# Performance work log

Measured on AMD Instinct MI355X. Metric: run time of the kernel, lower is better.

Reference implementation:

```python
import jax, jax.numpy as jnp
import numpy as np

B, S, H = 2, 2048, 2048
NH, NKV, HD = 16, 4, 128
LAT = H // 8  # compression_ratio=8


def _rope_tables():
    inv_freq = 1.0 / (10000.0 ** (jnp.arange(0, HD, 2, dtype=jnp.float32) / HD))
    pos = jnp.arange(S, dtype=jnp.float32)
    freqs = pos[:, None] * inv_freq[None, :]          # [S, HD/2]
    emb = jnp.concatenate([freqs, freqs], axis=-1)    # [S, HD]
    return jnp.cos(emb)[None, None], jnp.sin(emb)[None, None]  # [1,1,S,HD]


def setup_inputs() -> dict:
    key = jax.random.key(0)
    ks = jax.random.split(key, 8)
    std = 0.02
    hidden_states = jax.random.normal(ks[0], (B, S, H), dtype=jnp.float32)
    cos, sin = _rope_tables()
    # additive causal mask, broadcast over batch/heads
    causal = jnp.tril(jnp.ones((S, S), dtype=bool))
    attention_mask = jnp.where(causal, 0.0, -1e9).astype(jnp.float32)[None, None]
    Wq = jax.random.normal(ks[1], (H, H), dtype=jnp.float32) * std
    Wk = jax.random.normal(ks[2], (NKV * HD, H), dtype=jnp.float32) * std
    Wv = jax.random.normal(ks[3], (NKV * HD, H), dtype=jnp.float32) * std
    Wo = jax.random.normal(ks[4], (H, H), dtype=jnp.float32) * std
    Wl_in = jax.random.normal(ks[5], (LAT, H), dtype=jnp.float32) * std
    Wl_out = jax.random.normal(ks[6], (H, LAT), dtype=jnp.float32) * std
    latent_gate = jnp.ones((1,), dtype=jnp.float32)
    return dict(hidden_states=hidden_states, cos=cos, sin=sin,
                attention_mask=attention_mask, Wq=Wq, Wk=Wk, Wv=Wv, Wo=Wo,
                Wl_in=Wl_in, Wl_out=Wl_out, latent_gate=latent_gate)


def _rotate_half(x):
    x1, x2 = jnp.split(x, 2, axis=-1)
    return jnp.concatenate([-x2, x1], axis=-1)


def reference(hidden_states, cos, sin, attention_mask, Wq, Wk, Wv, Wo,
              Wl_in, Wl_out, latent_gate):
    b, s, h = hidden_states.shape
    # projections (torch Linear: x @ W.T)
    q = (hidden_states @ Wq.T).reshape(b, s, NH, HD).transpose(0, 2, 1, 3)    # [b,nh,s,hd]
    k = (hidden_states @ Wk.T).reshape(b, s, NKV, HD).transpose(0, 2, 1, 3)   # [b,nkv,s,hd]
    v = (hidden_states @ Wv.T).reshape(b, s, NKV, HD).transpose(0, 2, 1, 3)
    # inline RoPE
    c, sn = cos[:, :, :s, :], sin[:, :, :s, :]
    q = q * c + _rotate_half(q) * sn
    k = k * c + _rotate_half(k) * sn
    # GQA: replicate kv heads (repeat_interleave along head dim)
    rep = NH // NKV
    k = jnp.repeat(k, rep, axis=1)
    v = jnp.repeat(v, rep, axis=1)
    scores = jnp.einsum('bhqd,bhkd->bhqk', q, k) / np.sqrt(HD).astype(np.float32)
    scores = scores + attention_mask
    attn = jax.nn.softmax(scores, axis=-1)
    ctx = jnp.einsum('bhqk,bhkd->bhqd', attn, v)          # [b,nh,s,hd]
    ctx = ctx.transpose(0, 2, 1, 3).reshape(b, s, h)
    attn_out = ctx @ Wo.T
    latent = (hidden_states @ Wl_in.T) @ Wl_out.T          # low-rank residual branch
    return attn_out + latent_gate * latent
```

## Files before the change

kernel.cpp:

```cpp
#include <hip/hip_runtime.h>
#include <hip/hip_bf16.h>

#define Bn   2
#define Sn   2048
#define Hn   2048
#define NHn  16
#define NKVn 4
#define HDn  128
#define LATn 256
#define Mn   (Bn*Sn)
#define KC   2304

typedef unsigned short ushort_t;
typedef __attribute__((ext_vector_type(8))) short bf16x8;
typedef __attribute__((ext_vector_type(8))) unsigned short ushort8;
typedef __attribute__((ext_vector_type(4))) float f32x4;

__device__ __forceinline__ ushort_t f2bf(float f) {
    unsigned u = __float_as_uint(f);
    u += 0x7fffu + ((u >> 16) & 1u);
    return (ushort_t)(u >> 16);
}
__device__ __forceinline__ float bf2f(ushort_t h) {
    return __uint_as_float(((unsigned)h) << 16);
}
__device__ __forceinline__ void async16(const void* g, void* l) {
    __builtin_amdgcn_global_load_lds(
        (__attribute__((address_space(1))) void*)g,
        (__attribute__((address_space(3))) void*)l, 16, 0, 0);
}

struct CastArgs {
    const float* src[7];
    ushort_t*    dst[7];
    int n4[7];
    int sshift[7];
    int dcols[7];
    int dcoff[7];
};
__global__ __launch_bounds__(256)
void cast_fused(CastArgs a)
{
    int off = blockIdx.x * 256 + threadIdx.x;
    int seg = 0;
    while (seg < 6 && off >= a.n4[seg]) { off -= a.n4[seg]; ++seg; }
    const int r = off >> a.sshift[seg];
    const int c = off & ((1 << a.sshift[seg]) - 1);
    float4 f = ((const float4*)a.src[seg])[off];
    ushort4 o;
    o.x = f2bf(f.x); o.y = f2bf(f.y); o.z = f2bf(f.z); o.w = f2bf(f.w);
    ((ushort4*)a.dst[seg])[(size_t)r * a.dcols[seg] + a.dcoff[seg] + c] = o;
}

#define GEMM_BK64_LOOP(Aptr, Astr, Wptr, Wstr, Kdim)                          \
    for (int k0 = 0; k0 < (Kdim); k0 += 64) {                                 \
        _Pragma("unroll")                                                     \
        for (int it = 0; it < 4; ++it)                                        \
            async16((Aptr) + (size_t)(m0 + it*32 + srow)*(Astr) + k0 + scol,  \
                    As + (it*256 + tid)*8);                                   \
        _Pragma("unroll")                                                     \
        for (int it = 0; it < 4; ++it)                                        \
            async16((Wptr) + (size_t)(n0 + it*32 + srow)*(Wstr) + k0 + scol,  \
                    Bsm + (it*256 + tid)*8);                                  \
        __syncthreads();                                                      \
        _Pragma("unroll")                                                     \
        for (int hf = 0; hf < 2; ++hf) {                                      \
            bf16x8 af[4], bfr[4];                                             \
            _Pragma("unroll")                                                 \
            for (int mi = 0; mi < 4; ++mi)                                    \
                af[mi] = *(const bf16x8*)(As + aoff[hf*4 + mi]);              \
            _Pragma("unroll")                                                 \
            for (int ni = 0; ni < 4; ++ni)                                    \
                bfr[ni] = *(const bf16x8*)(Bsm + boff[hf*4 + ni]);            \
            _Pragma("unroll")                                                 \
            for (int mi = 0; mi < 4; ++mi)                                    \
                _Pragma("unroll")                                             \
                for (int ni = 0; ni < 4; ++ni)                                \
                    acc[mi][ni] = __builtin_amdgcn_mfma_f32_16x16x32_bf16(    \
                        af[mi], bfr[ni], acc[mi][ni], 0, 0, 0);               \
        }                                                                     \
        __syncthreads();                                                      \
    }

#define GEMM_COMMON_DECLS                                                     \
    const int tid  = threadIdx.x;                                             \
    const int lane = tid & 63, w = tid >> 6;                                  \
    const int t = lane & 15, q = lane >> 4;                                   \
    const int wm = w & 1, wn = w >> 1;                                        \
    const int srow = tid >> 3;                                                \
    const int scol = ((tid & 7) ^ ((tid >> 3) & 7)) * 8;                      \
    int aoff[8], boff[8];                                                     \
    _Pragma("unroll")                                                         \
    for (int hf = 0; hf < 2; ++hf)                                            \
        _Pragma("unroll")                                                     \
        for (int i = 0; i < 4; ++i) {                                         \
            aoff[hf*4 + i] = (wm*64 + i*16 + t)*64 + (((hf*4 + q) ^ (t & 7)) << 3); \
            boff[hf*4 + i] = (wn*64 + i*16 + t)*64 + (((hf*4 + q) ^ (t & 7)) << 3); \
        }                                                                     \
    f32x4 acc[4][4];                                                          \
    _Pragma("unroll")                                                         \
    for (int i = 0; i < 4; ++i)                                               \
        _Pragma("unroll")                                                     \
        for (int j = 0; j < 4; ++j) acc[i][j] = (f32x4){0.f, 0.f, 0.f, 0.f};

__global__ __launch_bounds__(256)
void gemm_qkv(const ushort_t* __restrict__ A, const ushort_t* __restrict__ W,
              ushort_t* __restrict__ qo, ushort_t* __restrict__ ko,
              ushort_t* __restrict__ vo)
{
    __shared__ __align__(16) ushort_t smem[16384];
    ushort_t* As  = smem;
    ushort_t* Bsm = smem + 8192;

    const int m0 = blockIdx.y * 128, n0 = blockIdx.x * 128;
    GEMM_COMMON_DECLS
    GEMM_BK64_LOOP(A, Hn, W, Hn, Hn)

    const int bidx = m0 >> 11, s0 = m0 & (Sn - 1);

    if (n0 >= 2560) {
        const int head = (n0 - 2560) >> 7;
        ushort_t* T = smem;
        #pragma unroll
        for (int h2 = 0; h2 < 2; ++h2) {
            __syncthreads();
            if (wn == h2) {
                #pragma unroll
                for (int mi = 0; mi < 4; ++mi)
                    #pragma unroll
                    for (int ni = 0; ni < 4; ++ni)
                        #pragma unroll
                        for (int r = 0; r < 4; ++r)
                            T[(wm*64 + mi*16 + q*4 + r)*64 + ni*16 + t] =
                                f2bf(acc[mi][ni][r]);
            }
            __syncthreads();
            const int dl = tid >> 2, tseg = (tid & 3) * 32;
            const size_t base =
                ((size_t)(bidx*NKVn + head)*HDn + h2*64 + dl) * Sn + s0 + tseg;
            #pragma unroll
            for (int j0 = 0; j0 < 4; ++j0) {
                ushort8 pk;
                #pragma unroll
                for (int u = 0; u < 8; ++u) pk[u] = T[(tseg + j0*8 + u)*64 + dl];
                *(ushort8*)(vo + base + j0*8) = pk;
            }
        }
        return;
    }

    ushort_t* outp;
    int hh;
    if (n0 < 2048) { outp = qo; hh = n0 >> 7; }
    else           { outp = ko; hh = (n0 - 2048) >> 7; }
    const int nheads = (n0 < 2048) ? NHn : NKVn;
    const size_t hbase = (((size_t)(bidx*nheads + hh))*Sn + s0) * HDn;

    #pragma unroll
    for (int mi = 0; mi < 4; ++mi)
        #pragma unroll
        for (int r = 0; r < 4; ++r) {
            const int sl = wm*64 + mi*16 + q*4 + r;
            #pragma unroll
            for (int ni = 0; ni < 4; ++ni) {
                const int d = wn*64 + ni*16 + t;
                outp[hbase + (size_t)sl*HDn + d] = f2bf(acc[mi][ni][r]);
            }
        }
}

template<int EPI>
__global__ __launch_bounds__(256)
void gemm_main(const ushort_t* __restrict__ A, const ushort_t* __restrict__ W,
               float* __restrict__ outf, ushort_t* __restrict__ outb,
               const float* __restrict__ gatep,
               int N, int K, int Astride, int Wstride, int OS)
{
    __shared__ __align__(16) ushort_t smem[16384];
    ushort_t* As  = smem;
    ushort_t* Bsm = smem + 8192;

    const int m0 = blockIdx.y * 128, n0 = blockIdx.x * 128;
    GEMM_COMMON_DECLS
    GEMM_BK64_LOOP(A, Astride, W, Wstride, K)

    float gate = 1.f;
    if (EPI == 2) gate = gatep[0];

    #pragma unroll
    for (int mi = 0; mi < 4; ++mi)
        #pragma unroll
        for (int r = 0; r < 4; ++r) {
            const int m = m0 + wm*64 + mi*16 + q*4 + r;
            #pragma unroll
            for (int ni = 0; ni < 4; ++ni) {
                const int n = n0 + wn*64 + ni*16 + t;
                const float v = acc[mi][ni][r];
                if (EPI == 0)      outf[(size_t)m * N + n] = v;
                else if (EPI == 2) outb[(size_t)m * OS + n] = f2bf(gate * v);
            }
        }
}

__global__ __launch_bounds__(256)
void rope2_bf16(ushort_t* __restrict__ qx, ushort_t* __restrict__ kx,
                const float* __restrict__ cosb, const float* __restrict__ sinb)
{
    const int gid = blockIdx.x * 256 + threadIdx.x;
    const int row = gid >> 6, d = gid & 63;
    ushort_t* x; int r;
    if (row < Bn*NHn*Sn) { x = qx; r = row; }
    else                 { x = kx; r = row - Bn*NHn*Sn; }
    const int s = r & (Sn - 1);
    const float c0 = cosb[s*HDn + d],      c1 = cosb[s*HDn + d + 64];
    const float s0 = sinb[s*HDn + d],      s1 = sinb[s*HDn + d + 64];
    const size_t base = (size_t)r * HDn;
    const float x0 = bf2f(x[base + d]), x1 = bf2f(x[base + d + 64]);
    x[base + d]      = f2bf(x0*c0 - x1*s0);
    x[base + d + 64] = f2bf(x1*c1 + x0*s1);
}

__global__ __launch_bounds__(256)
void attn_mfma(const ushort_t* __restrict__ qg, const ushort_t* __restrict__ kg,
               const ushort_t* __restrict__ vtg, ushort_t* __restrict__ ctxb)
{
    __shared__ __align__(16) ushort_t Ks[8192];
    __shared__ __align__(16) ushort_t Vt[8192];
    __shared__ __align__(16) ushort_t Ps[4096];

    const int tid = threadIdx.x;
    const int w = tid >> 6, lane = tid & 63;
    const int t = lane & 15, q = lane >> 4;
    const int bh = blockIdx.y;
    const int b = bh >> 4, h = bh & 15;
    const int kvh = h >> 2;
    const ushort_t* qhead  = qg  + ((size_t)(b*NHn  + h  ))*Sn*HDn;
    const ushort_t* khead  = kg  + ((size_t)(b*NKVn + kvh))*Sn*HDn;
    const ushort_t* vthead = vtg + ((size_t)(b*NKVn + kvh))*HDn*Sn;

    const int ksr = tid >> 4;
    const int ksb = (tid & 15) ^ (ksr & 15);
    const int vtr = tid >> 3;
    const int vtb = (tid & 7) ^ (vtr & 7);

    int aqo[4], bko[16], vto[16], pso[16];
    #pragma unroll
    for (int ks = 0; ks < 4; ++ks)
        aqo[ks] = (w*16 + t)*128 + (((ks*4 + q) ^ t) << 3);
    #pragma unroll
    for (int nb = 0; nb < 4; ++nb)
        #pragma unroll
        for (int ks = 0; ks < 4; ++ks)
            bko[nb*4 + ks] = (nb*16 + t)*128 + (((ks*4 + q) ^ t) << 3);
    #pragma unroll
    for (int d2 = 0; d2 < 8; ++d2)
        #pragma unroll
        for (int ksp = 0; ksp < 2; ++ksp)
            vto[d2*2 + ksp] = (d2*16 + t)*64 + (((ksp*4 + q) ^ (t & 7)) << 3);
    #pragma unroll
    for (int nb = 0; nb < 4; ++nb)
        #pragma unroll
        for (int r = 0; r < 4; ++r) {
            const int row = q*4 + r;
            pso[nb*4 + r] = row*64 + (((nb*2 + (t >> 3)) ^ (row & 7)) << 3) + (t & 7);
        }

    const float cexp2 = 0.12751744737492532f;
    ushort_t* Pw = Ps + w*1024;
    const int apo0 = t*64 + ((q ^ (t & 7)) << 3);
    const int apo1 = t*64 + (((4 + q) ^ (t & 7)) << 3);

    for (int rep = 0; rep < 2; ++rep) {
        const int qt = rep ? (31 - (int)blockIdx.x) : (int)blockIdx.x;

        __syncthreads();
        #pragma unroll
        for (int it = 0; it < 4; ++it)
            async16(qhead + (size_t)(qt*64 + it*16 + ksr)*HDn + ksb*8,
                    Ks + it*2048 + tid*8);
        __syncthreads();
        bf16x8 aq[4];
        #pragma unroll
        for (int ks = 0; ks < 4; ++ks) aq[ks] = *(const bf16x8*)(Ks + aqo[ks]);
        __syncthreads();

        float l_lane[4] = {0.f, 0.f, 0.f, 0.f};
        f32x4 O[8];
        #pragma unroll
        for (int d2 = 0; d2 < 8; ++d2) O[d2] = (f32x4){0.f, 0.f, 0.f, 0.f};

        for (int kt = 0; kt <= qt; ++kt) {
            #pragma unroll
            for (int it = 0; it < 4; ++it)
                async16(khead + (size_t)(kt*64 + it*16 + ksr)*HDn + ksb*8,
                        Ks + it*2048 + tid*8);
            #pragma unroll
            for (int it = 0; it < 4; ++it)
                async16(vthead + (size_t)(it*32 + vtr)*Sn + kt*64 + vtb*8,
                        Vt + it*2048 + tid*8);
            __syncthreads();

            f32x4 sc[4];
            #pragma unroll
            for (int nb = 0; nb < 4; ++nb) {
                sc[nb] = (f32x4){0.f, 0.f, 0.f, 0.f};
                #pragma unroll
                for (int ks = 0; ks < 4; ++ks) {
                    bf16x8 bk = *(const bf16x8*)(Ks + bko[nb*4 + ks]);
                    sc[nb] = __builtin_amdgcn_mfma_f32_16x16x32_bf16(
                        aq[ks], bk, sc[nb], 0, 0, 0);
                }
            }

            float ps[4][4];
            if (kt == qt) {
                #pragma unroll
                for (int nb = 0; nb < 4; ++nb) {
                    const int kj = kt*64 + nb*16 + t;
                    #pragma unroll
                    for (int r = 0; r < 4; ++r) {
                        const int qi = qt*64 + w*16 + q*4 + r;
                        ps[nb][r] = (kj <= qi) ? exp2f(sc[nb][r]*cexp2) : 0.f;
                    }
                }
            } else {
                #pragma unroll
                for (int nb = 0; nb < 4; ++nb)
                    #pragma unroll
                    for (int r = 0; r < 4; ++r)
                        ps[nb][r] = exp2f(sc[nb][r]*cexp2);
            }
            #pragma unroll
            for (int nb = 0; nb < 4; ++nb)
                #pragma unroll
                for (int r = 0; r < 4; ++r) {
                    l_lane[r] += ps[nb][r];
                    Pw[pso[nb*4 + r]] = f2bf(ps[nb][r]);
                }

            bf16x8 ap0 = *(const bf16x8*)(Pw + apo0);
            bf16x8 ap1 = *(const bf16x8*)(Pw + apo1);
            #pragma unroll
            for (int d2 = 0; d2 < 8; ++d2) {
                bf16x8 bv0 = *(const bf16x8*)(Vt + vto[d2*2 + 0]);
                O[d2] = __builtin_amdgcn_mfma_f32_16x16x32_bf16(ap0, bv0, O[d2], 0, 0, 0);
                bf16x8 bv1 = *(const bf16x8*)(Vt + vto[d2*2 + 1]);
                O[d2] = __builtin_amdgcn_mfma_f32_16x16x32_bf16(ap1, bv1, O[d2], 0, 0, 0);
            }
            __syncthreads();
        }

        float linv[4];
        #pragma unroll
        for (int r = 0; r < 4; ++r) {
            float lr = l_lane[r];
            lr += __shfl_xor(lr, 1);
            lr += __shfl_xor(lr, 2);
            lr += __shfl_xor(lr, 4);
            lr += __shfl_xor(lr, 8);
            linv[r] = 1.f / lr;
        }
        #pragma unroll
        for (int d2 = 0; d2 < 8; ++d2)
            #pragma unroll
            for (int r = 0; r < 4; ++r) {
                const size_t addr =
                    ((size_t)(b*Sn + qt*64 + w*16 + q*4 + r))*KC + h*HDn + d2*16 + t;
                ctxb[addr] = f2bf(O[d2][r] * linv[r]);
            }
    }
}

extern "C" void kernel_launch(void* const* d_in, const int* in_sizes, int n_in,
                              void* d_out, int out_size, void* d_ws, size_t ws_size,
                              hipStream_t stream)
{
    const float* hs    = (const float*)d_in[0];
    const float* cosb  = (const float*)d_in[1];
    const float* sinb  = (const float*)d_in[2];
    const float* Wq    = (const float*)d_in[4];
    const float* Wk    = (const float*)d_in[5];
    const float* Wv    = (const float*)d_in[6];
    const float* Wo    = (const float*)d_in[7];
    const float* Wlin  = (const float*)d_in[8];
    const float* Wlout = (const float*)d_in[9];
    const float* gate  = (const float*)d_in[10];
    float* out = (float*)d_out;

    ushort_t* p = (ushort_t*)d_ws;
    ushort_t* hsb    = p;  p += 8388608;
    ushort_t* Wqkvb  = p;  p += 3072*2048;
    ushort_t* Wcomb  = p;  p += 2048*KC;
    ushort_t* Wlinb  = p;  p += 524288;
    ushort_t* qbb    = p;  p += 8388608;
    ushort_t* kbb    = p;  p += 2097152;
    ushort_t* vtb    = p;  p += 2097152;
    ushort_t* ctxc   = p;  p += (size_t)Mn*KC;

    const dim3 blk(256);

    {
        CastArgs ca;
        ca.src[0]=hs;    ca.dst[0]=hsb;                 ca.n4[0]=2097152; ca.sshift[0]=21; ca.dcols[0]=1<<21; ca.dcoff[0]=0;
        ca.src[1]=Wq;    ca.dst[1]=Wqkvb;               ca.n4[1]=1048576; ca.sshift[1]=20; ca.dcols[1]=1<<20; ca.dcoff[1]=0;
        ca.src[2]=Wk;    ca.dst[2]=Wqkvb + 2048*2048;   ca.n4[2]=262144;  ca.sshift[2]=18; ca.dcols[2]=1<<18; ca.dcoff[2]=0;
        ca.src[3]=Wv;    ca.dst[3]=Wqkvb + 2560*2048;   ca.n4[3]=262144;  ca.sshift[3]=18; ca.dcols[3]=1<<18; ca.dcoff[3]=0;
        ca.src[4]=Wlin;  ca.dst[4]=Wlinb;               ca.n4[4]=131072;  ca.sshift[4]=17; ca.dcols[4]=1<<17; ca.dcoff[4]=0;
        ca.src[5]=Wo;    ca.dst[5]=Wcomb;               ca.n4[5]=1048576; ca.sshift[5]=9;  ca.dcols[5]=576;   ca.dcoff[5]=0;
        ca.src[6]=Wlout; ca.dst[6]=Wcomb;               ca.n4[6]=131072;  ca.sshift[6]=6;  ca.dcols[6]=576;   ca.dcoff[6]=512;
        cast_fused<<<19456, blk, 0, stream>>>(ca);
    }

    gemm_qkv<<<dim3(24, 32), blk, 0, stream>>>(hsb, Wqkvb, qbb, kbb, vtb);

    rope2_bf16<<<((Bn*NHn*Sn + Bn*NKVn*Sn)*64)/256, blk, 0, stream>>>(qbb, kbb, cosb, sinb);

    gemm_main<2><<<dim3(2, 32), blk, 0, stream>>>(hsb, Wlinb, nullptr, ctxc + 2048,
                                                  gate, LATn, Hn, Hn, Hn, KC);

    attn_mfma<<<dim3(16, Bn*NHn), blk, 0, stream>>>(qbb, kbb, vtb, ctxc);

    gemm_main<0><<<dim3(16, 32), blk, 0, stream>>>(ctxc, Wcomb, out, nullptr,
                                                   nullptr, Hn, KC, KC, KC, 0);
}
```

Measured before the change: 390.5 us.

## Fuse latent-in projection into QKV GEMM and double-buffer K tiles in attention

Appends Wl_in rows to the QKV weight so the latent-in projection is computed in the same GEMM launch, with a gated bf16 epilogue writing into the ctx concat buffer. This removes the separate small 64-block GEMM launch, which had poor occupancy. The attention kernel now double-buffers K tiles in LDS and prefetches the next K tile while computing the current one, moving the barrier after the P store. The cost is a second 16 KB K buffer in LDS, which may reduce occupancy, and V loads are still issued in the same iteration they are consumed.

Result: slower. 413.1 us (+5.8%).

```diff
diff --git a/kernel.cpp b/kernel.cpp
--- a/kernel.cpp
+++ b/kernel.cpp
@@ -10,6 +10,7 @@
 #define LATn 256
 #define Mn   (Bn*Sn)
 #define KC   2304
+#define NWn  3328
 
 typedef unsigned short ushort_t;
 typedef __attribute__((ext_vector_type(8))) short bf16x8;
@@ -106,7 +107,8 @@
 __global__ __launch_bounds__(256)
 void gemm_qkv(const ushort_t* __restrict__ A, const ushort_t* __restrict__ W,
               ushort_t* __restrict__ qo, ushort_t* __restrict__ ko,
-              ushort_t* __restrict__ vo)
+              ushort_t* __restrict__ vo, ushort_t* __restrict__ ctxb,
+              const float* __restrict__ gatep)
 {
     __shared__ __align__(16) ushort_t smem[16384];
     ushort_t* As  = smem;
@@ -117,6 +119,23 @@
     GEMM_BK64_LOOP(A, Hn, W, Hn, Hn)
 
     const int bidx = m0 >> 11, s0 = m0 & (Sn - 1);
+
+    if (n0 >= 3072) {
+        const float gate = gatep[0];
+        const int c0 = 2048 + (n0 - 3072);
+        #pragma unroll
+        for (int mi = 0; mi < 4; ++mi)
+            #pragma unroll
+            for (int r = 0; r < 4; ++r) {
+                const int m = m0 + wm*64 + mi*16 + q*4 + r;
+                #pragma unroll
+                for (int ni = 0; ni < 4; ++ni) {
+                    const int n = c0 + wn*64 + ni*16 + t;
+                    ctxb[(size_t)m * KC + n] = f2bf(gate * acc[mi][ni][r]);
+                }
+            }
+        return;
+    }
 
     if (n0 >= 2560) {
         const int head = (n0 - 2560) >> 7;
@@ -169,12 +188,9 @@
         }
 }
 
-template<int EPI>
 __global__ __launch_bounds__(256)
-void gemm_main(const ushort_t* __restrict__ A, const ushort_t* __restrict__ W,
-               float* __restrict__ outf, ushort_t* __restrict__ outb,
-               const float* __restrict__ gatep,
-               int N, int K, int Astride, int Wstride, int OS)
+void gemm_out(const ushort_t* __restrict__ A, const ushort_t* __restrict__ W,
+              float* __restrict__ outf)
 {
     __shared__ __align__(16) ushort_t smem[16384];
     ushort_t* As  = smem;
@@ -182,10 +198,7 @@
 
     const int m0 = blockIdx.y * 128, n0 = blockIdx.x * 128;
     GEMM_COMMON_DECLS
-    GEMM_BK64_LOOP(A, Astride, W, Wstride, K)
-
-    float gate = 1.f;
-    if (EPI == 2) gate = gatep[0];
+    GEMM_BK64_LOOP(A, KC, W, KC, KC)
 
     #pragma unroll
     for (int mi = 0; mi < 4; ++mi)
@@ -195,9 +208,7 @@
             #pragma unroll
             for (int ni = 0; ni < 4; ++ni) {
                 const int n = n0 + wn*64 + ni*16 + t;
-                const float v = acc[mi][ni][r];
-                if (EPI == 0)      outf[(size_t)m * N + n] = v;
-                else if (EPI == 2) outb[(size_t)m * OS + n] = f2bf(gate * v);
+                outf[(size_t)m * Hn + n] = acc[mi][ni][r];
             }
         }
 }
@@ -224,7 +235,7 @@
 void attn_mfma(const ushort_t* __restrict__ qg, const ushort_t* __restrict__ kg,
                const ushort_t* __restrict__ vtg, ushort_t* __restrict__ ctxb)
 {
-    __shared__ __align__(16) ushort_t Ks[8192];
+    __shared__ __align__(16) ushort_t Ks[2][8192];
     __shared__ __align__(16) ushort_t Vt[8192];
     __shared__ __align__(16) ushort_t Ps[4096];
 
@@ -277,11 +288,17 @@
         #pragma unroll
         for (int it = 0; it < 4; ++it)
             async16(qhead + (size_t)(qt*64 + it*16 + ksr)*HDn + ksb*8,
-                    Ks + it*2048 + tid*8);
+                    Ks[0] + it*2048 + tid*8);
         __syncthreads();
         bf16x8 aq[4];
         #pragma unroll
-        for (int ks = 0; ks < 4; ++ks) aq[ks] = *(const bf16x8*)(Ks + aqo[ks]);
+        for (int ks = 0; ks < 4; ++ks) aq[ks] = *(const bf16x8*)(Ks[0] + aqo[ks]);
+        __syncthreads();
+
+        #pragma unroll
+        for (int it = 0; it < 4; ++it)
+            async16(khead + (size_t)(it*16 + ksr)*HDn + ksb*8,
+                    Ks[0] + it*2048 + tid*8);
         __syncthreads();
 
         float l_lane[4] = {0.f, 0.f, 0.f, 0.f};
@@ -290,15 +307,19 @@
         for (int d2 = 0; d2 < 8; ++d2) O[d2] = (f32x4){0.f, 0.f, 0.f, 0.f};
 
         for (int kt = 0; kt <= qt; ++kt) {
-            #pragma unroll
-            for (int it = 0; it < 4; ++it)
-                async16(khead + (size_t)(kt*64 + it*16 + ksr)*HDn + ksb*8,
-                        Ks + it*2048 + tid*8);
+            const ushort_t* Kc = Ks[kt & 1];
+            ushort_t*       Kn = Ks[(kt & 1) ^ 1];
+
             #pragma unroll
             for (int it = 0; it < 4; ++it)
                 async16(vthead + (size_t)(it*32 + vtr)*Sn + kt*64 + vtb*8,
                         Vt + it*2048 + tid*8);
-            __syncthreads();
+            if (kt < qt) {
+                #pragma unroll
+                for (int it = 0; it < 4; ++it)
+                    async16(khead + (size_t)((kt+1)*64 + it*16 + ksr)*HDn + ksb*8,
+                            Kn + it*2048 + tid*8);
+            }
 
             f32x4 sc[4];
             #pragma unroll
@@ -306,7 +327,7 @@
                 sc[nb] = (f32x4){0.f, 0.f, 0.f, 0.f};
                 #pragma unroll
                 for (int ks = 0; ks < 4; ++ks) {
-                    bf16x8 bk = *(const bf16x8*)(Ks + bko[nb*4 + ks]);
+                    bf16x8 bk = *(const bf16x8*)(Kc + bko[nb*4 + ks]);
                     sc[nb] = __builtin_amdgcn_mfma_f32_16x16x32_bf16(
                         aq[ks], bk, sc[nb], 0, 0, 0);
                 }
@@ -337,6 +358,8 @@
                     l_lane[r] += ps[nb][r];
                     Pw[pso[nb*4 + r]] = f2bf(ps[nb][r]);
                 }
+
+            __syncthreads();
 
             bf16x8 ap0 = *(const bf16x8*)(Pw + apo0);
             bf16x8 ap1 = *(const bf16x8*)(Pw + apo1);
@@ -389,9 +412,8 @@
 
     ushort_t* p = (ushort_t*)d_ws;
     ushort_t* hsb    = p;  p += 8388608;
-    ushort_t* Wqkvb  = p;  p += 3072*2048;
+    ushort_t* Wqkvb  = p;  p += (size_t)NWn*2048;
     ushort_t* Wcomb  = p;  p += 2048*KC;
-    ushort_t* Wlinb  = p;  p += 524288;
     ushort_t* qbb    = p;  p += 8388608;
     ushort_t* kbb    = p;  p += 2097152;
     ushort_t* vtb    = p;  p += 2097152;
@@ -405,21 +427,17 @@
         ca.src[1]=Wq;    ca.dst[1]=Wqkvb;               ca.n4[1]=1048576; ca.sshift[1]=20; ca.dcols[1]=1<<20; ca.dcoff[1]=0;
         ca.src[2]=Wk;    ca.dst[2]=Wqkvb + 2048*2048;   ca.n4[2]=262144;  ca.sshift[2]=18; ca.dcols[2]=1<<18; ca.dcoff[2]=0;
         ca.src[3]=Wv;    ca.dst[3]=Wqkvb + 2560*2048;   ca.n4[3]=262144;  ca.sshift[3]=18; ca.dcols[3]=1<<18; ca.dcoff[3]=0;
-        ca.src[4]=Wlin;  ca.dst[4]=Wlinb;               ca.n4[4]=131072;  ca.sshift[4]=17; ca.dcols[4]=1<<17; ca.dcoff[4]=0;
+        ca.src[4]=Wlin;  ca.dst[4]=Wqkvb + 3072*2048;   ca.n4[4]=131072;  ca.sshift[4]=17; ca.dcols[4]=1<<17; ca.dcoff[4]=0;
         ca.src[5]=Wo;    ca.dst[5]=Wcomb;               ca.n4[5]=1048576; ca.sshift[5]=9;  ca.dcols[5]=576;   ca.dcoff[5]=0;
         ca.src[6]=Wlout; ca.dst[6]=Wcomb;               ca.n4[6]=131072;  ca.sshift[6]=6;  ca.dcols[6]=576;   ca.dcoff[6]=512;
         cast_fused<<<19456, blk, 0, stream>>>(ca);
     }
 
-    gemm_qkv<<<dim3(24, 32), blk, 0, stream>>>(hsb, Wqkvb, qbb, kbb, vtb);
+    gemm_qkv<<<dim3(26, 32), blk, 0, stream>>>(hsb, Wqkvb, qbb, kbb, vtb, ctxc, gate);
 
     rope2_bf16<<<((Bn*NHn*Sn + Bn*NKVn*Sn)*64)/256, blk, 0, stream>>>(qbb, kbb, cosb, sinb);
 
-    gemm_main<2><<<dim3(2, 32), blk, 0, stream>>>(hsb, Wlinb, nullptr, ctxc + 2048,
-                                                  gate, LATn, Hn, Hn, Hn, KC);
-
     attn_mfma<<<dim3(16, Bn*NHn), blk, 0, stream>>>(qbb, kbb, vtb, ctxc);
 
-    gemm_main<0><<<dim3(16, 32), blk, 0, stream>>>(ctxc, Wcomb, out, nullptr,
-                                                   nullptr, Hn, KC, KC, KC, 0);
-}
+    gemm_out<<<dim3(16, 32), blk, 0, stream>>>(ctxc, Wcomb, out);
+}
```
